# Kernel tuning notes

Hardware: AMD Instinct MI355X
Metric: run time of the kernel (lower is better)

The kernel has to match this reference:

```python
import jax, jax.numpy as jnp
import numpy as np

B, S, D, H = 2, 4096, 768, 12
DEPTH = D // H


def setup_inputs() -> dict:
    key = jax.random.key(0)
    ks = jax.random.split(key, 6)
    return {
        "q": jax.random.normal(ks[0], (B, S, D), dtype=jnp.float32),
        "k": jax.random.normal(ks[1], (B, S, D), dtype=jnp.float32),
        "v": jax.random.normal(ks[2], (B, S, D), dtype=jnp.float32),
        "wq": jax.random.normal(ks[3], (D, D), dtype=jnp.float32),
        "wk": jax.random.normal(ks[4], (D, D), dtype=jnp.float32),
        "wv": jax.random.normal(ks[5], (D, D), dtype=jnp.float32),
    }


def _split_heads(x):
    # [B, S, D] -> [B, H, S, depth]
    b, s, _ = x.shape
    return x.reshape(b, s, H, DEPTH).transpose(0, 2, 1, 3)


def reference(q, k, v, wq, wk, wv):
    qh = _split_heads(q @ wq)  # [B,H,S,dh]
    kh = _split_heads(k @ wk)
    vh = _split_heads(v @ wv)
    scale = 1.0 / jnp.sqrt(jnp.asarray(DEPTH, dtype=qh.dtype))
    scores = jnp.einsum("bhqd,bhkd->bhqk", qh, kh) * scale  # [B,H,S,S]
    attn = jax.nn.softmax(scores, axis=-1)
    out = jnp.einsum("bhqk,bhkd->bhqd", attn, vh)  # [B,H,S,dh]
    return out.transpose(0, 2, 1, 3).reshape(q.shape[0], -1, D)
```

## Files before the change

### kernel.cpp

```cpp
#include <hip/hip_runtime.h>
#include <cstdint>

#define B_   2
#define S_   4096
#define D_   768
#define H_   12
#define DH_  64
#define BH_  (B_*H_)
#define M_   (B_*S_)
#define SCALE 0.125f

typedef _Float16 fp16;
typedef __attribute__((ext_vector_type(8))) _Float16 fp16x8;
typedef __attribute__((ext_vector_type(4))) _Float16 fp16x4;
typedef __attribute__((ext_vector_type(4))) float    f32x4;

#define MFMA16(a,b,c) __builtin_amdgcn_mfma_f32_16x16x32_f16((a),(b),(c),0,0,0)

__device__ __forceinline__ void gld_lds16(const void* g, void* l) {
  __builtin_amdgcn_global_load_lds(
      (const __attribute__((address_space(1))) unsigned int*)g,
      (__attribute__((address_space(3))) unsigned int*)l, 16, 0, 0);
}

__device__ __forceinline__ void stage64x128(const char* gbase, int pitch,
                                            char* lds, int tid) {
  const int lane = tid & 63, wv = tid >> 6;
#pragma unroll
  for (int j = 0; j < 2; ++j) {
    const int o   = (wv*2 + j)*1024 + lane*16;
    const int row = o >> 7;
    const int cb  = (o & 127) ^ ((row & 7) << 4);
    gld_lds16(gbase + (size_t)row*pitch + cb, lds + (wv*2 + j)*1024);
  }
}

__device__ __forceinline__ fp16x8 lds_h8(const char* base, int row, int cb) {
  return *(const fp16x8*)(base + row*128 + (cb ^ ((row & 7) << 4)));
}

__global__ __launch_bounds__(256) void prep_w(const float* __restrict__ wq,
                                              const float* __restrict__ wk,
                                              const float* __restrict__ wv,
                                              fp16* __restrict__ wt) {
  const int idx = blockIdx.x*256 + threadIdx.x;
  const int mat = idx / (768*768);
  const int e   = idx % (768*768);
  const int n   = e / 768, k = e % 768;
  const float* w = mat == 0 ? wq : (mat == 1 ? wk : wv);
  const float v = w[(size_t)k*768 + n];
  fp16* base = wt + (size_t)mat * (2*768*768);
  const fp16 hv = (fp16)v;
  base[e]            = hv;
  base[768*768 + e]  = (fp16)(v - (float)hv);
}

__global__ __launch_bounds__(256) void proj_gemm(
    const float* __restrict__ xq, const float* __restrict__ xk,
    const float* __restrict__ xv, const fp16* __restrict__ wt,
    fp16* __restrict__ qhi, fp16* __restrict__ qlo,
    fp16* __restrict__ khi, fp16* __restrict__ klo,
    fp16* __restrict__ vtp) {
  __shared__ __align__(16) char sm[16384];
  char* sWh = sm;
  char* sWl = sm + 8192;
  const int tid = threadIdx.x, lane = tid & 63, wv = tid >> 6;
  const int c = lane & 15, g = lane >> 4;
  const int mb  = blockIdx.x * 64;
  const int h   = blockIdx.y;
  const int nb  = h * 64;
  const int mat = blockIdx.z;
  const float* x = mat == 0 ? xq : (mat == 1 ? xk : xv);
  const fp16* wth = wt + (size_t)mat * (2*768*768);
  const fp16* wtl = wth + 768*768;

  f32x4 acc[4] = {};
  const int xrow = mb + wv*16 + c;

  for (int k0 = 0; k0 < 768; k0 += 64) {
    __syncthreads();
    stage64x128((const char*)(wth + (size_t)nb*768 + k0), 768*2, sWh, tid);
    stage64x128((const char*)(wtl + (size_t)nb*768 + k0), 768*2, sWl, tid);
    __syncthreads();

    fp16x8 ah[2], al[2];
#pragma unroll
    for (int ks = 0; ks < 2; ++ks) {
      const float* xp = x + (size_t)xrow*768 + k0 + ks*32 + g*8;
      const f32x4 x0 = *(const f32x4*)xp;
      const f32x4 x1 = *(const f32x4*)(xp + 4);
#pragma unroll
      for (int j = 0; j < 8; ++j) {
        const float v = j < 4 ? x0[j] : x1[j - 4];
        const fp16 hv = (fp16)v;
        ah[ks][j] = hv;
        al[ks][j] = (fp16)(v - (float)hv);
      }
    }
#pragma unroll
    for (int ks = 0; ks < 2; ++ks)
#pragma unroll
      for (int nt = 0; nt < 4; ++nt) {
        const fp16x8 bh = lds_h8(sWh, nt*16 + c, ks*64 + g*16);
        const fp16x8 bl = lds_h8(sWl, nt*16 + c, ks*64 + g*16);
        acc[nt] = MFMA16(ah[ks], bh, acc[nt]);
        acc[nt] = MFMA16(ah[ks], bl, acc[nt]);
        acc[nt] = MFMA16(al[ks], bh, acc[nt]);
      }
  }

  if (mat < 2) {
    fp16* ph = mat ? khi : qhi;
    fp16* pl = mat ? klo : qlo;
#pragma unroll
    for (int nt = 0; nt < 4; ++nt)
#pragma unroll
      for (int r = 0; r < 4; ++r) {
        const int m = mb + wv*16 + g*4 + r;
        const int bb = m >> 12, s = m & (S_-1);
        const size_t idx = ((size_t)(bb*H_ + h)*S_ + s)*DH_ + nt*16 + c;
        const float v = acc[nt][r];
        const fp16 hv = (fp16)v;
        ph[idx] = hv;
        pl[idx] = (fp16)(v - (float)hv);
      }
  } else {
    __syncthreads();
    fp16* tile = (fp16*)sm;
#pragma unroll
    for (int nt = 0; nt < 4; ++nt) {
      const int dd = nt*16 + c, ml = wv*16 + g*4;
      const fp16x4 hv = {(fp16)acc[nt][0], (fp16)acc[nt][1],
                         (fp16)acc[nt][2], (fp16)acc[nt][3]};
      *(fp16x4*)(tile + dd*64 + ml) = hv;
    }
    __syncthreads();
    const int bb = mb >> 12, s0 = mb & (S_-1);
    const int dd = tid >> 2, ml0 = (tid & 3) * 16;
    const size_t obase = ((size_t)(bb*H_ + h)*DH_ + dd)*S_ + s0 + ml0;
#pragma unroll
    for (int u = 0; u < 2; ++u)
      *(fp16x8*)(vtp + obase + u*8) = *(const fp16x8*)(tile + dd*64 + ml0 + u*8);
  }
}

__global__ __launch_bounds__(256) void mha_flash(
    const fp16* __restrict__ qhi, const fp16* __restrict__ qlo,
    const fp16* __restrict__ khi, const fp16* __restrict__ klo,
    const fp16* __restrict__ vt, float* __restrict__ out) {
  __shared__ __align__(16) char sm[49152];
  char* sQh = sm;
  char* sQl = sm + 8192;
  char* sKh = sm + 16384;
  char* sKl = sm + 24576;
  char* sV  = sm + 32768;
  char* sP  = sm + 40960;

  const int tid = threadIdx.x, lane = tid & 63, wv = tid >> 6;
  const int c = lane & 15, g = lane >> 4;
  const int qb = blockIdx.x * 64;
  const int bh = blockIdx.y;
  const int b = bh / H_, h = bh % H_;

  const size_t qoff = ((size_t)bh*S_ + qb) * DH_;
  stage64x128((const char*)(qhi + qoff), 128, sQh, tid);
  stage64x128((const char*)(qlo + qoff), 128, sQl, tid);
  __syncthreads();

  fp16x8 qfh[2], qfl[2];
#pragma unroll
  for (int ks = 0; ks < 2; ++ks) {
    qfh[ks] = lds_h8(sQh, wv*16 + c, ks*64 + g*16);
    qfl[ks] = lds_h8(sQl, wv*16 + c, ks*64 + g*16);
  }

  float m_run = -1e30f, l_run = 0.f;
  f32x4 accO[4] = {};

  for (int kt = 0; kt < S_/64; ++kt) {
    const int kvb = kt * 64;
    __syncthreads();
    const size_t koff = ((size_t)bh*S_ + kvb) * DH_;
    stage64x128((const char*)(khi + koff), 128, sKh, tid);
    stage64x128((const char*)(klo + koff), 128, sKl, tid);
    stage64x128((const char*)(vt + (size_t)bh*DH_*S_ + kvb), S_*2, sV, tid);
    __syncthreads();

    f32x4 accS[4] = {};
#pragma unroll
    for (int t = 0; t < 4; ++t)
#pragma unroll
      for (int ks = 0; ks < 2; ++ks) {
        const fp16x8 kfh = lds_h8(sKh, t*16 + c, ks*64 + g*16);
        const fp16x8 kfl = lds_h8(sKl, t*16 + c, ks*64 + g*16);
        accS[t] = MFMA16(kfh, qfh[ks], accS[t]);
        accS[t] = MFMA16(kfh, qfl[ks], accS[t]);
        accS[t] = MFMA16(kfl, qfh[ks], accS[t]);
      }

    float mx = -1e30f;
#pragma unroll
    for (int t = 0; t < 4; ++t)
#pragma unroll
      for (int r = 0; r < 4; ++r) mx = fmaxf(mx, accS[t][r]);
    mx = fmaxf(mx, __shfl_xor(mx, 16));
    mx = fmaxf(mx, __shfl_xor(mx, 32));
    const float m_new = fmaxf(m_run, mx);
    const float corr = __expf((m_run - m_new) * SCALE);
    float psum = 0.f;
#pragma unroll
    for (int t = 0; t < 4; ++t)
#pragma unroll
      for (int r = 0; r < 4; ++r) {
        const float p = __expf((accS[t][r] - m_new) * SCALE);
        accS[t][r] = p;
        psum += p;
      }
    psum += __shfl_xor(psum, 16);
    psum += __shfl_xor(psum, 32);
    l_run = l_run * corr + psum;
    m_run = m_new;

    char* pbase = sP + wv*2048;
#pragma unroll
    for (int t = 0; t < 4; ++t) {
      const fp16x4 pw = {(fp16)accS[t][0], (fp16)accS[t][1],
                         (fp16)accS[t][2], (fp16)accS[t][3]};
      *(fp16x4*)(pbase + c*128 + ((t*32 + g*8) ^ ((c & 7) << 4))) = pw;
    }

    float cr[4];
#pragma unroll
    for (int r = 0; r < 4; ++r)
      cr[r] = __shfl(corr, (lane & 48) | (g*4 + r));
#pragma unroll
    for (int d = 0; d < 4; ++d)
#pragma unroll
      for (int r = 0; r < 4; ++r) accO[d][r] *= cr[r];

#pragma unroll
    for (int ks = 0; ks < 2; ++ks) {
      const fp16x8 pf = *(const fp16x8*)(pbase + c*128 +
                                         ((ks*64 + g*16) ^ ((c & 7) << 4)));
#pragma unroll
      for (int d = 0; d < 4; ++d) {
        const fp16x8 vf = lds_h8(sV, d*16 + c, ks*64 + g*16);
        accO[d] = MFMA16(pf, vf, accO[d]);
      }
    }
  }

  float inv[4];
#pragma unroll
  for (int r = 0; r < 4; ++r)
    inv[r] = 1.f / __shfl(l_run, (lane & 48) | (g*4 + r));
  const int s0 = qb + wv*16 + g*4;
#pragma unroll
  for (int d = 0; d < 4; ++d)
#pragma unroll
    for (int r = 0; r < 4; ++r)
      out[((size_t)(b*S_ + s0 + r))*D_ + h*DH_ + d*16 + c] = accO[d][r] * inv[r];
}

extern "C" void kernel_launch(void* const* d_in, const int* in_sizes, int n_in,
                              void* d_out, int out_size, void* d_ws, size_t ws_size,
                              hipStream_t stream) {
  const float* xq = (const float*)d_in[0];
  const float* xk = (const float*)d_in[1];
  const float* xv = (const float*)d_in[2];
  const float* wq = (const float*)d_in[3];
  const float* wk = (const float*)d_in[4];
  const float* wv = (const float*)d_in[5];
  float* out = (float*)d_out;

  fp16* wt  = (fp16*)d_ws;
  fp16* qhi = wt + (size_t)6*768*768;
  const size_t PL = (size_t)BH_*S_*DH_;
  fp16* qlo = qhi + PL;
  fp16* khi = qlo + PL;
  fp16* klo = khi + PL;
  fp16* vtp = klo + PL;

  hipLaunchKernelGGL(prep_w, dim3(3*768*768/256), dim3(256), 0, stream,
                     wq, wk, wv, wt);
  hipLaunchKernelGGL(proj_gemm, dim3(M_/64, H_, 3), dim3(256), 0, stream,
                     xq, xk, xv, wt, qhi, qlo, khi, klo, vtp);
  hipLaunchKernelGGL(mha_flash, dim3(S_/64, BH_), dim3(256), 0, stream,
                     qhi, qlo, khi, klo, vtp, out);
}
```

Baseline: 524.2 us.

## Pre-split inputs to fp16 hi/lo, LDS-stage projection A, use hardware exp2

Adds a prep kernel that splits each fp32 input into fp16 hi/lo planes once, and a new projection GEMM that stages both X and W tiles in LDS instead of converting X per tile in registers. The path is used only when the workspace is large enough; otherwise the old fused kernel runs. The flash kernel reuses the Q staging buffers for K to shrink LDS from 48KB to 32KB, precomputes swizzle offsets, and replaces __expf with a raw v_exp_f32 on scale*log2e-folded FMAs. In exchange it adds extra global traffic and six more kernel launches for the X round trip.

After: 545.9 us. 4.1% more time.

```diff
diff --git a/kernel.cpp b/kernel.cpp
--- a/kernel.cpp
+++ b/kernel.cpp
@@ -17,6 +17,10 @@
 
 #define MFMA16(a,b,c) __builtin_amdgcn_mfma_f32_16x16x32_f16((a),(b),(c),0,0,0)
 
+__device__ __forceinline__ float exp2_hw(float x) {
+  float r; asm("v_exp_f32 %0, %1" : "=v"(r) : "v"(x)); return r;
+}
+
 __device__ __forceinline__ void gld_lds16(const void* g, void* l) {
   __builtin_amdgcn_global_load_lds(
       (const __attribute__((address_space(1))) unsigned int*)g,
@@ -33,10 +37,6 @@
     const int cb  = (o & 127) ^ ((row & 7) << 4);
     gld_lds16(gbase + (size_t)row*pitch + cb, lds + (wv*2 + j)*1024);
   }
-}
-
-__device__ __forceinline__ fp16x8 lds_h8(const char* base, int row, int cb) {
-  return *(const fp16x8*)(base + row*128 + (cb ^ ((row & 7) << 4)));
 }
 
 __global__ __launch_bounds__(256) void prep_w(const float* __restrict__ wq,
@@ -55,6 +55,107 @@
   base[768*768 + e]  = (fp16)(v - (float)hv);
 }
 
+__global__ __launch_bounds__(256) void prep_x(const float* __restrict__ x,
+                                              fp16* __restrict__ xh,
+                                              fp16* __restrict__ xl) {
+  const size_t i = ((size_t)blockIdx.x*256 + threadIdx.x) * 8;
+  const f32x4 a = *(const f32x4*)(x + i);
+  const f32x4 b = *(const f32x4*)(x + i + 4);
+  fp16x8 hv, lv;
+#pragma unroll
+  for (int j = 0; j < 8; ++j) {
+    const float v = j < 4 ? a[j] : b[j - 4];
+    const fp16 h = (fp16)v;
+    hv[j] = h; lv[j] = (fp16)(v - (float)h);
+  }
+  *(fp16x8*)(xh + i) = hv;
+  *(fp16x8*)(xl + i) = lv;
+}
+
+__global__ __launch_bounds__(256) void proj_gemmA(
+    const fp16* __restrict__ xh, const fp16* __restrict__ xl,
+    const fp16* __restrict__ wth,
+    fp16* __restrict__ ph, fp16* __restrict__ pl,
+    fp16* __restrict__ vtp, int isV) {
+  __shared__ __align__(16) char sm[32768];
+  char* sXh = sm;
+  char* sXl = sm + 8192;
+  char* sWh = sm + 16384;
+  char* sWl = sm + 24576;
+  const fp16* wtl = wth + 768*768;
+  const int tid = threadIdx.x, lane = tid & 63, wv = tid >> 6;
+  const int c = lane & 15, g = lane >> 4;
+  const int r128 = c * 128;
+  const int co0 = ((c & 7) ^ g) << 4;
+  const int co1 = co0 ^ 64;
+  const int mb  = blockIdx.x * 64;
+  const int h   = blockIdx.y;
+  const int nb  = h * 64;
+
+  f32x4 acc[4] = {};
+  for (int k0 = 0; k0 < 768; k0 += 64) {
+    __syncthreads();
+    stage64x128((const char*)(xh  + (size_t)mb*768 + k0), 1536, sXh, tid);
+    stage64x128((const char*)(xl  + (size_t)mb*768 + k0), 1536, sXl, tid);
+    stage64x128((const char*)(wth + (size_t)nb*768 + k0), 1536, sWh, tid);
+    stage64x128((const char*)(wtl + (size_t)nb*768 + k0), 1536, sWl, tid);
+    __syncthreads();
+
+    const int arow = (wv*16 + c) * 128;
+    const fp16x8 ah0 = *(const fp16x8*)(sXh + arow + co0);
+    const fp16x8 ah1 = *(const fp16x8*)(sXh + arow + co1);
+    const fp16x8 al0 = *(const fp16x8*)(sXl + arow + co0);
+    const fp16x8 al1 = *(const fp16x8*)(sXl + arow + co1);
+#pragma unroll
+    for (int nt = 0; nt < 4; ++nt) {
+      const char* wb  = sWh + r128 + nt*2048;
+      const char* wlb = sWl + r128 + nt*2048;
+      const fp16x8 bh0 = *(const fp16x8*)(wb  + co0);
+      const fp16x8 bh1 = *(const fp16x8*)(wb  + co1);
+      const fp16x8 bl0 = *(const fp16x8*)(wlb + co0);
+      const fp16x8 bl1 = *(const fp16x8*)(wlb + co1);
+      acc[nt] = MFMA16(ah0, bh0, acc[nt]);
+      acc[nt] = MFMA16(ah0, bl0, acc[nt]);
+      acc[nt] = MFMA16(al0, bh0, acc[nt]);
+      acc[nt] = MFMA16(ah1, bh1, acc[nt]);
+      acc[nt] = MFMA16(ah1, bl1, acc[nt]);
+      acc[nt] = MFMA16(al1, bh1, acc[nt]);
+    }
+  }
+
+  if (!isV) {
+#pragma unroll
+    for (int nt = 0; nt < 4; ++nt)
+#pragma unroll
+      for (int r = 0; r < 4; ++r) {
+        const int m = mb + wv*16 + g*4 + r;
+        const int bb = m >> 12, s = m & (S_-1);
+        const size_t idx = ((size_t)(bb*H_ + h)*S_ + s)*DH_ + nt*16 + c;
+        const float v = acc[nt][r];
+        const fp16 hv = (fp16)v;
+        ph[idx] = hv;
+        pl[idx] = (fp16)(v - (float)hv);
+      }
+  } else {
+    __syncthreads();
+    fp16* tile = (fp16*)sm;
+#pragma unroll
+    for (int nt = 0; nt < 4; ++nt) {
+      const int dd = nt*16 + c, ml = wv*16 + g*4;
+      const fp16x4 hv = {(fp16)acc[nt][0], (fp16)acc[nt][1],
+                         (fp16)acc[nt][2], (fp16)acc[nt][3]};
+      *(fp16x4*)(tile + dd*64 + ml) = hv;
+    }
+    __syncthreads();
+    const int bb = mb >> 12, s0 = mb & (S_-1);
+    const int dd = tid >> 2, ml0 = (tid & 3) * 16;
+    const size_t obase = ((size_t)(bb*H_ + h)*DH_ + dd)*S_ + s0 + ml0;
+#pragma unroll
+    for (int u = 0; u < 2; ++u)
+      *(fp16x8*)(vtp + obase + u*8) = *(const fp16x8*)(tile + dd*64 + ml0 + u*8);
+  }
+}
+
 __global__ __launch_bounds__(256) void proj_gemm(
     const float* __restrict__ xq, const float* __restrict__ xk,
     const float* __restrict__ xv, const fp16* __restrict__ wt,
@@ -66,6 +167,9 @@
   char* sWl = sm + 8192;
   const int tid = threadIdx.x, lane = tid & 63, wv = tid >> 6;
   const int c = lane & 15, g = lane >> 4;
+  const int r128 = c * 128;
+  const int co0 = ((c & 7) ^ g) << 4;
+  const int co1 = co0 ^ 64;
   const int mb  = blockIdx.x * 64;
   const int h   = blockIdx.y;
   const int nb  = h * 64;
@@ -79,8 +183,8 @@
 
   for (int k0 = 0; k0 < 768; k0 += 64) {
     __syncthreads();
-    stage64x128((const char*)(wth + (size_t)nb*768 + k0), 768*2, sWh, tid);
-    stage64x128((const char*)(wtl + (size_t)nb*768 + k0), 768*2, sWl, tid);
+    stage64x128((const char*)(wth + (size_t)nb*768 + k0), 1536, sWh, tid);
+    stage64x128((const char*)(wtl + (size_t)nb*768 + k0), 1536, sWl, tid);
     __syncthreads();
 
     fp16x8 ah[2], al[2];
@@ -101,8 +205,11 @@
     for (int ks = 0; ks < 2; ++ks)
 #pragma unroll
       for (int nt = 0; nt < 4; ++nt) {
-        const fp16x8 bh = lds_h8(sWh, nt*16 + c, ks*64 + g*16);
-        const fp16x8 bl = lds_h8(sWl, nt*16 + c, ks*64 + g*16);
+        const char* wb  = sWh + r128 + nt*2048;
+        const char* wlb = sWl + r128 + nt*2048;
+        const int co = ks ? co1 : co0;
+        const fp16x8 bh = *(const fp16x8*)(wb  + co);
+        const fp16x8 bl = *(const fp16x8*)(wlb + co);
         acc[nt] = MFMA16(ah[ks], bh, acc[nt]);
         acc[nt] = MFMA16(ah[ks], bl, acc[nt]);
         acc[nt] = MFMA16(al[ks], bh, acc[nt]);
@@ -148,71 +255,82 @@
     const fp16* __restrict__ qhi, const fp16* __restrict__ qlo,
     const fp16* __restrict__ khi, const fp16* __restrict__ klo,
     const fp16* __restrict__ vt, float* __restrict__ out) {
-  __shared__ __align__(16) char sm[49152];
-  char* sQh = sm;
-  char* sQl = sm + 8192;
-  char* sKh = sm + 16384;
-  char* sKl = sm + 24576;
-  char* sV  = sm + 32768;
-  char* sP  = sm + 40960;
+  __shared__ __align__(16) char sm[32768];
+  char* sKh = sm;
+  char* sKl = sm + 8192;
+  char* sV  = sm + 16384;
+  char* sP  = sm + 24576;
 
   const int tid = threadIdx.x, lane = tid & 63, wv = tid >> 6;
   const int c = lane & 15, g = lane >> 4;
+  const int r128 = c * 128;
+  const int co0 = ((c & 7) ^ g) << 4;
+  const int co1 = co0 ^ 64;
+  const int pg3 = (g & 1) << 3;
+  const int pse = ((c & 7) ^ (g >> 1)) << 4;
   const int qb = blockIdx.x * 64;
   const int bh = blockIdx.y;
   const int b = bh / H_, h = bh % H_;
 
   const size_t qoff = ((size_t)bh*S_ + qb) * DH_;
-  stage64x128((const char*)(qhi + qoff), 128, sQh, tid);
-  stage64x128((const char*)(qlo + qoff), 128, sQl, tid);
+  stage64x128((const char*)(qhi + qoff), 128, sKh, tid);
+  stage64x128((const char*)(qlo + qoff), 128, sKl, tid);
   __syncthreads();
 
   fp16x8 qfh[2], qfl[2];
-#pragma unroll
-  for (int ks = 0; ks < 2; ++ks) {
-    qfh[ks] = lds_h8(sQh, wv*16 + c, ks*64 + g*16);
-    qfl[ks] = lds_h8(sQl, wv*16 + c, ks*64 + g*16);
+  {
+    const int qrow = (wv*16 + c) * 128;
+    qfh[0] = *(const fp16x8*)(sKh + qrow + co0);
+    qfh[1] = *(const fp16x8*)(sKh + qrow + co1);
+    qfl[0] = *(const fp16x8*)(sKl + qrow + co0);
+    qfl[1] = *(const fp16x8*)(sKl + qrow + co1);
   }
 
   float m_run = -1e30f, l_run = 0.f;
   f32x4 accO[4] = {};
+  const float C2 = 0.125f * 1.4426950408889634f;
 
   for (int kt = 0; kt < S_/64; ++kt) {
-    const int kvb = kt * 64;
-    __syncthreads();
-    const size_t koff = ((size_t)bh*S_ + kvb) * DH_;
+    __syncthreads();
+    const size_t koff = ((size_t)bh*S_ + kt*64) * DH_;
     stage64x128((const char*)(khi + koff), 128, sKh, tid);
     stage64x128((const char*)(klo + koff), 128, sKl, tid);
-    stage64x128((const char*)(vt + (size_t)bh*DH_*S_ + kvb), S_*2, sV, tid);
+    stage64x128((const char*)(vt + (size_t)bh*DH_*S_ + kt*64), S_*2, sV, tid);
     __syncthreads();
 
     f32x4 accS[4] = {};
 #pragma unroll
+    for (int t = 0; t < 4; ++t) {
+      const char* kb = sKh + r128 + t*2048;
+      const char* lb = sKl + r128 + t*2048;
+      const fp16x8 kh0 = *(const fp16x8*)(kb + co0);
+      const fp16x8 kh1 = *(const fp16x8*)(kb + co1);
+      const fp16x8 kl0 = *(const fp16x8*)(lb + co0);
+      const fp16x8 kl1 = *(const fp16x8*)(lb + co1);
+      accS[t] = MFMA16(kh0, qfh[0], accS[t]);
+      accS[t] = MFMA16(kh0, qfl[0], accS[t]);
+      accS[t] = MFMA16(kl0, qfh[0], accS[t]);
+      accS[t] = MFMA16(kh1, qfh[1], accS[t]);
+      accS[t] = MFMA16(kh1, qfl[1], accS[t]);
+      accS[t] = MFMA16(kl1, qfh[1], accS[t]);
+    }
+
+    float mx = -1e30f;
+#pragma unroll
     for (int t = 0; t < 4; ++t)
-#pragma unroll
-      for (int ks = 0; ks < 2; ++ks) {
-        const fp16x8 kfh = lds_h8(sKh, t*16 + c, ks*64 + g*16);
-        const fp16x8 kfl = lds_h8(sKl, t*16 + c, ks*64 + g*16);
-        accS[t] = MFMA16(kfh, qfh[ks], accS[t]);
-        accS[t] = MFMA16(kfh, qfl[ks], accS[t]);
-        accS[t] = MFMA16(kfl, qfh[ks], accS[t]);
-      }
-
-    float mx = -1e30f;
-#pragma unroll
-    for (int t = 0; t < 4; ++t)
-#pragma unroll
-      for (int r = 0; r < 4; ++r) mx = fmaxf(mx, accS[t][r]);
+      mx = fmaxf(mx, fmaxf(fmaxf(accS[t][0], accS[t][1]),
+                           fmaxf(accS[t][2], accS[t][3])));
     mx = fmaxf(mx, __shfl_xor(mx, 16));
     mx = fmaxf(mx, __shfl_xor(mx, 32));
     const float m_new = fmaxf(m_run, mx);
-    const float corr = __expf((m_run - m_new) * SCALE);
+    const float nm = m_new * C2;
+    const float corr = exp2_hw(__builtin_fmaf(m_run, C2, -nm));
     float psum = 0.f;
 #pragma unroll
     for (int t = 0; t < 4; ++t)
 #pragma unroll
       for (int r = 0; r < 4; ++r) {
-        const float p = __expf((accS[t][r] - m_new) * SCALE);
+        const float p = exp2_hw(__builtin_fmaf(accS[t][r], C2, -nm));
         accS[t][r] = p;
         psum += p;
       }
@@ -221,12 +339,12 @@
     l_run = l_run * corr + psum;
     m_run = m_new;
 
-    char* pbase = sP + wv*2048;
+    char* pbase = sP + wv*2048 + r128;
 #pragma unroll
     for (int t = 0; t < 4; ++t) {
       const fp16x4 pw = {(fp16)accS[t][0], (fp16)accS[t][1],
                          (fp16)accS[t][2], (fp16)accS[t][3]};
-      *(fp16x4*)(pbase + c*128 + ((t*32 + g*8) ^ ((c & 7) << 4))) = pw;
+      *(fp16x4*)(pbase + (pg3 | (pse ^ (t*32)))) = pw;
     }
 
     float cr[4];
@@ -238,15 +356,13 @@
 #pragma unroll
       for (int r = 0; r < 4; ++r) accO[d][r] *= cr[r];
 
-#pragma unroll
-    for (int ks = 0; ks < 2; ++ks) {
-      const fp16x8 pf = *(const fp16x8*)(pbase + c*128 +
-                                         ((ks*64 + g*16) ^ ((c & 7) << 4)));
-#pragma unroll
-      for (int d = 0; d < 4; ++d) {
-        const fp16x8 vf = lds_h8(sV, d*16 + c, ks*64 + g*16);
-        accO[d] = MFMA16(pf, vf, accO[d]);
-      }
+    const fp16x8 pf0 = *(const fp16x8*)(pbase + co0);
+    const fp16x8 pf1 = *(const fp16x8*)(pbase + co1);
+#pragma unroll
+    for (int d = 0; d < 4; ++d) {
+      const char* vb = sV + r128 + d*2048;
+      accO[d] = MFMA16(pf0, *(const fp16x8*)(vb + co0), accO[d]);
+      accO[d] = MFMA16(pf1, *(const fp16x8*)(vb + co1), accO[d]);
     }
   }
 
@@ -280,11 +396,28 @@
   fp16* khi = qlo + PL;
   fp16* klo = khi + PL;
   fp16* vtp = klo + PL;
+  fp16* xh  = vtp + PL;
+  fp16* xl  = xh + (size_t)M_*D_;
+  const size_t need = (size_t)((char*)(xl + (size_t)M_*D_) - (char*)d_ws);
 
   hipLaunchKernelGGL(prep_w, dim3(3*768*768/256), dim3(256), 0, stream,
                      wq, wk, wv, wt);
-  hipLaunchKernelGGL(proj_gemm, dim3(M_/64, H_, 3), dim3(256), 0, stream,
-                     xq, xk, xv, wt, qhi, qlo, khi, klo, vtp);
+
+  if (ws_size >= need) {
+    for (int mat = 0; mat < 3; ++mat) {
+      const float* x = mat == 0 ? xq : (mat == 1 ? xk : xv);
+      hipLaunchKernelGGL(prep_x, dim3((M_*D_)/(256*8)), dim3(256), 0, stream,
+                         x, xh, xl);
+      hipLaunchKernelGGL(proj_gemmA, dim3(M_/64, H_), dim3(256), 0, stream,
+                         xh, xl, wt + (size_t)mat*2*768*768,
+                         mat == 1 ? khi : qhi, mat == 1 ? klo : qlo,
+                         vtp, mat == 2 ? 1 : 0);
+    }
+  } else {
+    hipLaunchKernelGGL(proj_gemm, dim3(M_/64, H_, 3), dim3(256), 0, stream,
+                       xq, xk, xv, wt, qhi, qlo, khi, klo, vtp);
+  }
+
   hipLaunchKernelGGL(mha_flash, dim3(S_/64, BH_), dim3(256), 0, stream,
                      qhi, qlo, khi, klo, vtp, out);
 }
```
